# Optimization experiments

Measured on AMD Instinct MI355X. Metric: run time of the kernel, lower is better.

## Reference

```python
import jax, jax.numpy as jnp
import numpy as np

NUM_USER = 200000
NUM_QUESTION = 20000
NUM_CONCEPT = 128
DIM_HIDDEN = 512
BATCH = 16384


def _build_graph():
    # Deterministic DAG: edges go from lower to higher concept index, so
    # topological order is 0..C-1. Edge list is ordered by (to, from), so the
    # predecessors of node k occupy a contiguous slice of edge indices, matching
    # know_graph[know_graph['to']==k].sort_values(by='from').index.
    rng = np.random.RandomState(0)
    preds, offs, e = [], [], 0
    for k in range(NUM_CONCEPT):
        lp = 0 if k == 0 else int(rng.randint(0, min(k, 3) + 1))
        p = sorted(rng.choice(k, size=lp, replace=False).tolist()) if lp > 0 else []
        preds.append(p)
        offs.append(e)
        e += lp
    return preds, offs, e

PREDS, OFFS, NUM_EDGE = _build_graph()


def setup_inputs() -> dict:
    key = jax.random.key(0)
    ks = jax.random.split(key, 16)
    h2 = max(DIM_HIDDEN // 2, 1)
    inp = {
        'user_id': jax.random.randint(ks[0], (BATCH,), 0, NUM_USER),
        'question_id': jax.random.randint(ks[1], (BATCH,), 0, NUM_QUESTION),
        'priori': jax.random.normal(ks[2], (NUM_USER, NUM_CONCEPT), jnp.float32) * 0.1,
        'condi_p': jax.random.normal(ks[3], (NUM_USER, NUM_EDGE), jnp.float32) * 0.1,
        'condi_n': jax.random.normal(ks[4], (NUM_USER, NUM_EDGE), jnp.float32) * 0.1,
        'item_diff': jax.random.normal(ks[5], (NUM_QUESTION, NUM_CONCEPT), jnp.float32) * 0.1,
        'item_disc': jax.random.normal(ks[6], (NUM_QUESTION, 1), jnp.float32) * 0.1,
        'q_table': (jax.random.uniform(ks[7], (NUM_QUESTION, NUM_CONCEPT)) < 0.1).astype(jnp.float32),
        'Wu': jax.random.normal(ks[8], (DIM_HIDDEN, NUM_CONCEPT), jnp.float32) * 0.05,
        'bu': jnp.zeros((DIM_HIDDEN,), jnp.float32),
        'Wi': jax.random.normal(ks[9], (DIM_HIDDEN, NUM_CONCEPT), jnp.float32) * 0.05,
        'bi': jnp.zeros((DIM_HIDDEN,), jnp.float32),
        'W1': jax.random.normal(ks[10], (h2, DIM_HIDDEN), jnp.float32) * 0.05,
        'b1': jnp.zeros((h2,), jnp.float32),
        'W2': jax.random.normal(ks[11], (1, h2), jnp.float32) * 0.05,
        'b2': jnp.zeros((1,), jnp.float32),
    }
    return inp


def _posterior(user_id, priori, condi_p, condi_n):
    bp = jax.nn.sigmoid(priori[user_id])   # [B, C]
    bcp = jax.nn.sigmoid(condi_p[user_id])  # [B, E]
    bcn = jax.nn.sigmoid(condi_n[user_id])  # [B, E]
    post = [None] * NUM_CONCEPT
    for k in range(NUM_CONCEPT):
        preds = PREDS[k]
        lp = len(preds)
        if lp == 0:
            post[k] = bp[:, k]
            continue
        pr = jnp.stack([post[p] for p in preds], axis=1)          # [B, lp]
        cp = bcp[:, OFFS[k]:OFFS[k] + lp] ** (1.0 / lp)           # [B, lp]
        cn = bcn[:, OFFS[k]:OFFS[k] + lp] ** (1.0 / lp)
        # Exact closed form of the 2^lp mask sum: sum over binary masks of
        # prod_j(m_j*cp_j*pr_j + (1-m_j)*cn_j*(1-pr_j)) = prod_j(cp_j*pr_j + cn_j*(1-pr_j))
        post[k] = jnp.prod(cp * pr + cn * (1.0 - pr), axis=1)
    return jnp.stack(post, axis=1)  # [B, C]


def reference(user_id, question_id, priori, condi_p, condi_n, item_diff, item_disc,
              q_table, Wu, bu, Wi, bi, W1, b1, W2, b2):
    user_mastery = _posterior(user_id, priori, condi_p, condi_n)      # [B, C]
    diff = jax.nn.sigmoid(item_diff[question_id])                     # [B, C]
    disc = jax.nn.sigmoid(item_disc[question_id])                     # [B, 1]
    q = q_table[question_id]                                          # [B, C]
    user_factor = jnp.tanh((user_mastery * q) @ Wu.T + bu)            # [B, H]
    item_factor = jax.nn.sigmoid((diff * q) @ Wi.T + bi)              # [B, H]
    x = (user_factor - item_factor) * disc
    x = jax.nn.sigmoid(x @ W1.T + b1)
    x = jax.nn.sigmoid(x @ W2.T + b2)                                 # [B, 1]
    return jnp.squeeze(x, axis=-1)
```

## Files before the change

### kernel.cpp

```cpp
#include <hip/hip_runtime.h>
#include <hip/hip_bf16.h>
#include <stdint.h>

typedef __hip_bfloat16 bf16;

struct GraphArg {
  short offs[128];
  unsigned char lp[128];
  unsigned char preds[384];
  unsigned char elp[384];
};

namespace {
struct HostMT {
  uint32_t mt[624]; int pos;
  void seed(uint32_t s){
    mt[0]=s;
    for(int i=1;i<624;i++) mt[i]=1812433253u*(mt[i-1]^(mt[i-1]>>30))+(uint32_t)i;
    pos=624;
  }
  uint32_t next(){
    if(pos>=624){
      for(int i=0;i<624;i++){
        uint32_t y=(mt[i]&0x80000000u)|(mt[(i+1)%624]&0x7fffffffu);
        mt[i]=mt[(i+397)%624]^(y>>1)^((y&1u)?0x9908b0dfu:0u);
      }
      pos=0;
    }
    uint32_t y=mt[pos++];
    y^=y>>11; y^=(y<<7)&0x9d2c5680u; y^=(y<<15)&0xefc60000u; y^=y>>18;
    return y;
  }
  uint64_t next64(){ uint64_t hi=next(); uint64_t lo=next(); return (hi<<32)|lo; }
  uint32_t masked32(uint32_t rng){
    if(!rng) return 0u;
    uint32_t mask=rng; mask|=mask>>1; mask|=mask>>2; mask|=mask>>4; mask|=mask>>8; mask|=mask>>16;
    uint32_t v; do{ v=next()&mask; }while(v>rng); return v;
  }
  uint64_t masked64(uint64_t rng){
    if(!rng) return 0ull;
    uint64_t mask=rng; mask|=mask>>1; mask|=mask>>2; mask|=mask>>4; mask|=mask>>8; mask|=mask>>16; mask|=mask>>32;
    uint64_t v; do{ v=next64()&mask; }while(v>rng); return v;
  }
};

int build_graph(GraphArg& g, bool rand64, bool shuf64){
  HostMT st; st.seed(0u);
  for(int j=0;j<384;j++) g.elp[j]=0;
  int e=0; int perm[128];
  for(int k=0;k<128;k++){
    int l=0;
    if(k>0){
      uint32_t rng=(uint32_t)(k<3?k:3);
      l = rand64 ? (int)st.masked64(rng) : (int)st.masked32(rng);
    }
    g.offs[k]=(short)e; g.lp[k]=(unsigned char)l;
    g.preds[k*3]=0; g.preds[k*3+1]=0; g.preds[k*3+2]=0;
    if(l>0){
      for(int i=0;i<k;i++) perm[i]=i;
      for(int i=k-1;i>=1;i--){
        uint32_t j = shuf64 ? (uint32_t)st.masked64((uint64_t)i) : st.masked32((uint32_t)i);
        int t=perm[i]; perm[i]=perm[j]; perm[j]=t;
      }
      int sel[3]; for(int j=0;j<l;j++) sel[j]=perm[j];
      for(int a=1;a<l;a++){ int v=sel[a]; int b=a-1; while(b>=0&&sel[b]>v){sel[b+1]=sel[b];b--;} sel[b+1]=v; }
      for(int j=0;j<l;j++){ g.preds[k*3+j]=(unsigned char)sel[j]; g.elp[e+j]=(unsigned char)l; }
    }
    e+=l;
  }
  return e;
}
}

__device__ __forceinline__ float bf2f(bf16 v){ return __bfloat162float(v); }
__device__ __forceinline__ float sigmoidf_(float x){ return 1.0f/(1.0f+expf(-x)); }

template<bool F32> __device__ __forceinline__ float ld1(const void* p, long long i){
  if constexpr(F32) return ((const float*)p)[i];
  else return bf2f(((const bf16*)p)[i]);
}
template<bool F32> __device__ __forceinline__ void ld8(const void* p, long long i, float* f){
  if constexpr(F32){
    const float4* q = (const float4*)((const float*)p + i);
    float4 a=q[0], b=q[1];
    f[0]=a.x; f[1]=a.y; f[2]=a.z; f[3]=a.w; f[4]=b.x; f[5]=b.y; f[6]=b.z; f[7]=b.w;
  } else {
    union { uint4 u; unsigned short s[8]; } x;
    x.u = *reinterpret_cast<const uint4*>((const bf16*)p + i);
#pragma unroll
    for(int j=0;j<8;j++){ unsigned uu=((unsigned)x.s[j])<<16; float ff; __builtin_memcpy(&ff,&uu,4); f[j]=ff; }
  }
}
template<bool F32> __device__ __forceinline__ void st1(void* p, long long i, float v){
  if constexpr(F32) ((float*)p)[i]=v;
  else ((bf16*)p)[i]=__float2bfloat16(v);
}

__device__ __forceinline__ int pidx(int k,int e){ return (k<<4) + (e ^ (k&15)); }

template<bool F32>
__global__ __launch_bounds__(256) void fused(
    const int* __restrict__ user_id, const int* __restrict__ question_id,
    const void* __restrict__ priori, const void* __restrict__ condi_p, const void* __restrict__ condi_n,
    const void* __restrict__ item_diff, const void* __restrict__ item_disc, const void* __restrict__ q_table,
    const void* __restrict__ Wu, const void* __restrict__ bu,
    const void* __restrict__ Wi, const void* __restrict__ bi,
    const void* __restrict__ W1, const void* __restrict__ b1,
    const void* __restrict__ W2, const void* __restrict__ b2,
    void* __restrict__ out, long long E, long long maxCondi, GraphArg g)
{
  {
    const unsigned short* ph = (const unsigned short*)priori;
    int cnt=0;
#pragma unroll
    for(int i=0;i<64;i++){ unsigned ex=(ph[i]>>7)&0xFFu; cnt += (ex>=0x82u)?1:0; }
    const bool isF32 = (cnt>=4);
    if(isF32 != F32) return;
  }

  __shared__ __align__(16) char arena[40960];
  float* s_dq  =(float*)(arena);
  float* s_post=(float*)(arena+8192);
  float* s_cp  =(float*)(arena+16384);
  float* s_cn  =(float*)(arena+26880);
  float* s_mq  =(float*)(arena+16384);
  float* s_x   =(float*)(arena+24576);
  float* s_x1  =(float*)(arena+8192);

  const int tid=threadIdx.x;
  const long long b0=(long long)blockIdx.x*16;
  const int Ei=(int)E;
  const bool staged=(Ei>0 && Ei<=164);

  float qv[8];
#pragma unroll
  for(int it=0;it<8;++it){
    const int i=tid+(it<<8);
    const int e=i>>7, c=i&127;
    const int u=user_id[b0+e];
    s_post[pidx(c,e)]=sigmoidf_(ld1<F32>(priori,(long long)u*128+c));
    const int q=question_id[b0+e];
    const float qvv=ld1<F32>(q_table,(long long)q*128+c);
    qv[it]=qvv;
    s_dq[e*128+c]=sigmoidf_(ld1<F32>(item_diff,(long long)q*128+c))*qvv;
  }
  if(staged && tid<Ei){
    const int j=tid, lp=(int)g.elp[j];
    for(int e=0;e<16;e++){
      const int u=user_id[b0+e];
      const long long idx=(long long)u*E+j;
      float cp=sigmoidf_(ld1<F32>(condi_p,idx));
      float cn=sigmoidf_(ld1<F32>(condi_n,idx));
      if(lp==2){cp=sqrtf(cp);cn=sqrtf(cn);}
      else if(lp==3){cp=cbrtf(cp);cn=cbrtf(cn);}
      s_cp[e*Ei+j]=cp; s_cn[e*Ei+j]=cn;
    }
  }
  __syncthreads();

  if(tid<16){
    const int e=tid;
    if(staged){
      for(int k=0;k<128;k++){
        const int lp=(int)g.lp[k];
        if(lp==0) continue;
        const int off=(int)g.offs[k];
        float prod=1.0f;
        for(int j=0;j<lp;j++){
          const float pr=s_post[pidx((int)g.preds[k*3+j],e)];
          prod*=s_cp[e*Ei+off+j]*pr + s_cn[e*Ei+off+j]*(1.0f-pr);
        }
        s_post[pidx(k,e)]=prod;
      }
    } else {
      const int u=user_id[b0+e];
      const long long ubase=(long long)u*E;
      for(int k=0;k<128;k++){
        const int lp=(int)g.lp[k];
        if(lp==0) continue;
        const int off=(int)g.offs[k];
        float prod=1.0f;
        for(int j=0;j<lp;j++){
          long long idx=ubase+off+j; if(idx>maxCondi) idx=maxCondi;
          float bcp=sigmoidf_(ld1<F32>(condi_p,idx));
          float bcn=sigmoidf_(ld1<F32>(condi_n,idx));
          float cp,cn;
          if(lp==1){cp=bcp;cn=bcn;}
          else if(lp==2){cp=sqrtf(bcp);cn=sqrtf(bcn);}
          else {cp=cbrtf(bcp);cn=cbrtf(bcn);}
          const float pr=s_post[pidx((int)g.preds[k*3+j],e)];
          prod*=cp*pr+cn*(1.0f-pr);
        }
        s_post[pidx(k,e)]=prod;
      }
    }
  }
  __syncthreads();

#pragma unroll
  for(int it=0;it<8;++it){
    const int i=tid+(it<<8);
    const int e=i>>7, c=i&127;
    s_mq[e*128+c]=s_post[pidx(c,e)]*qv[it];
  }
  __syncthreads();

  for(int tile=0;tile<2;tile++){
    const int e0=tile*8;
    float dsc[8];
#pragma unroll
    for(int e=0;e<8;e++){
      const int q=question_id[b0+e0+e];
      dsc[e]=sigmoidf_(ld1<F32>(item_disc,q));
    }
    for(int half=0;half<2;half++){
      const int o=tid+half*256;
      float aU[8],aI[8];
#pragma unroll
      for(int e=0;e<8;e++){aU[e]=0.0f;aI[e]=0.0f;}
      for(int c=0;c<128;c+=8){
        float u8[8],i8[8];
        ld8<F32>(Wu,(long long)o*128+c,u8);
        ld8<F32>(Wi,(long long)o*128+c,i8);
#pragma unroll
        for(int e=0;e<8;e++){
          const float* m=&s_mq[(e0+e)*128+c];
          const float* d=&s_dq[(e0+e)*128+c];
#pragma unroll
          for(int j=0;j<8;j++){ aU[e]+=u8[j]*m[j]; aI[e]+=i8[j]*d[j]; }
        }
      }
      const float bou=ld1<F32>(bu,o), boi=ld1<F32>(bi,o);
#pragma unroll
      for(int e=0;e<8;e++){
        float uf=tanhf(aU[e]+bou);
        float fi=sigmoidf_(aI[e]+boi);
        s_x[e*512+o]=(uf-fi)*dsc[e];
      }
    }
    __syncthreads();
    {
      float a[8];
#pragma unroll
      for(int e=0;e<8;e++) a[e]=0.0f;
      for(int c=0;c<512;c+=8){
        float w8[8]; ld8<F32>(W1,(long long)tid*512+c,w8);
#pragma unroll
        for(int e=0;e<8;e++){
          const float* x=&s_x[e*512+c];
#pragma unroll
          for(int j=0;j<8;j++) a[e]+=w8[j]*x[j];
        }
      }
      const float bb=ld1<F32>(b1,tid);
#pragma unroll
      for(int e=0;e<8;e++) s_x1[e*256+tid]=sigmoidf_(a[e]+bb);
    }
    __syncthreads();
    {
      const int e=tid>>5, l=tid&31;
      float a=0.0f;
      for(int h=l;h<256;h+=32) a+=s_x1[e*256+h]*ld1<F32>(W2,h);
      for(int off=16;off>0;off>>=1) a+=__shfl_down(a,off,32);
      if(l==0) st1<F32>(out,b0+e0+e,sigmoidf_(a+ld1<F32>(b2,0)));
    }
    __syncthreads();
  }
}

extern "C" void kernel_launch(void* const* d_in, const int* in_sizes, int n_in,
                              void* d_out, int out_size, void* d_ws, size_t ws_size,
                              hipStream_t stream) {
  const int* user_id     = (const int*)d_in[0];
  const int* question_id = (const int*)d_in[1];
  const void* priori     = d_in[2];
  const void* condi_p    = d_in[3];
  const void* condi_n    = d_in[4];
  const void* item_diff  = d_in[5];
  const void* item_disc  = d_in[6];
  const void* q_table    = d_in[7];
  const void* Wu = d_in[8];  const void* bu = d_in[9];
  const void* Wi = d_in[10]; const void* bi = d_in[11];
  const void* W1 = d_in[12]; const void* b1 = d_in[13];
  const void* W2 = d_in[14]; const void* b2 = d_in[15];
  (void)n_in; (void)out_size; (void)d_ws; (void)ws_size;

  const int batch    = in_sizes[0];
  const int num_user = in_sizes[2] / 128;
  const long long E  = in_sizes[3] / num_user;
  const long long maxCondi = (long long)num_user * E - 1;

  GraphArg g;
  int e_tot = build_graph(g, false, false);
  if(e_tot != (int)E) e_tot = build_graph(g, true,  false);
  if(e_tot != (int)E) e_tot = build_graph(g, false, true);
  if(e_tot != (int)E) e_tot = build_graph(g, true,  true);
  if(e_tot != (int)E) (void)build_graph(g, false, false);

  const int blocks = batch / 16;
  fused<false><<<blocks,256,0,stream>>>(user_id,question_id,priori,condi_p,condi_n,
      item_diff,item_disc,q_table,Wu,bu,Wi,bi,W1,b1,W2,b2,d_out,E,maxCondi,g);
  fused<true ><<<blocks,256,0,stream>>>(user_id,question_id,priori,condi_p,condi_n,
      item_diff,item_disc,q_table,Wu,bu,Wi,bi,W1,b1,W2,b2,d_out,E,maxCondi,g);
}
```

Measured before the change: 935.7 us.

## Process 32 batch rows per block and restructure shared-memory staging

Each block now handles 32 samples instead of 16, so the posterior recurrence runs on 32 lanes and the weight loads for Wu/Wi/W1 are reused across four 8-row tiles instead of two. The shared-memory arena grows to about 57KB with a new layout: the swizzled posterior index is replaced by a plain c*32+e layout, and the q_table/item_diff/item_disc loads move after the posterior phase. This halves the block count and raises shared memory per block, which may lower occupancy and parallelism across CUs.

New measurement: 757.3 us. -19.1%, faster.

```diff
diff --git a/kernel.cpp b/kernel.cpp
--- a/kernel.cpp
+++ b/kernel.cpp
@@ -95,8 +95,6 @@
   if constexpr(F32) ((float*)p)[i]=v;
   else ((bf16*)p)[i]=__float2bfloat16(v);
 }
-
-__device__ __forceinline__ int pidx(int k,int e){ return (k<<4) + (e ^ (k&15)); }
 
 template<bool F32>
 __global__ __launch_bounds__(256) void fused(
@@ -118,35 +116,29 @@
     if(isF32 != F32) return;
   }
 
-  __shared__ __align__(16) char arena[40960];
-  float* s_dq  =(float*)(arena);
-  float* s_post=(float*)(arena+8192);
+  __shared__ __align__(16) char arena[58368];
+  float* s_post=(float*)(arena);
+  float* s_x   =(float*)(arena);
+  float* s_x1  =(float*)(arena+16384);
   float* s_cp  =(float*)(arena+16384);
-  float* s_cn  =(float*)(arena+26880);
-  float* s_mq  =(float*)(arena+16384);
-  float* s_x   =(float*)(arena+24576);
-  float* s_x1  =(float*)(arena+8192);
+  float* s_disc=(float*)(arena+24576);
+  float* s_mq  =(float*)(arena+25600);
+  float* s_cn  =(float*)(arena+37376);
+  float* s_dq  =(float*)(arena+41984);
 
   const int tid=threadIdx.x;
-  const long long b0=(long long)blockIdx.x*16;
+  const long long b0=(long long)blockIdx.x*32;
   const int Ei=(int)E;
   const bool staged=(Ei>0 && Ei<=164);
 
-  float qv[8];
-#pragma unroll
-  for(int it=0;it<8;++it){
-    const int i=tid+(it<<8);
+  for(int i=tid;i<32*128;i+=256){
     const int e=i>>7, c=i&127;
     const int u=user_id[b0+e];
-    s_post[pidx(c,e)]=sigmoidf_(ld1<F32>(priori,(long long)u*128+c));
-    const int q=question_id[b0+e];
-    const float qvv=ld1<F32>(q_table,(long long)q*128+c);
-    qv[it]=qvv;
-    s_dq[e*128+c]=sigmoidf_(ld1<F32>(item_diff,(long long)q*128+c))*qvv;
+    s_post[c*32+e]=sigmoidf_(ld1<F32>(priori,(long long)u*128+c));
   }
   if(staged && tid<Ei){
     const int j=tid, lp=(int)g.elp[j];
-    for(int e=0;e<16;e++){
+    for(int e=0;e<32;e++){
       const int u=user_id[b0+e];
       const long long idx=(long long)u*E+j;
       float cp=sigmoidf_(ld1<F32>(condi_p,idx));
@@ -158,7 +150,7 @@
   }
   __syncthreads();
 
-  if(tid<16){
+  if(tid<32){
     const int e=tid;
     if(staged){
       for(int k=0;k<128;k++){
@@ -167,10 +159,10 @@
         const int off=(int)g.offs[k];
         float prod=1.0f;
         for(int j=0;j<lp;j++){
-          const float pr=s_post[pidx((int)g.preds[k*3+j],e)];
+          const float pr=s_post[(int)g.preds[k*3+j]*32+e];
           prod*=s_cp[e*Ei+off+j]*pr + s_cn[e*Ei+off+j]*(1.0f-pr);
         }
-        s_post[pidx(k,e)]=prod;
+        s_post[k*32+e]=prod;
       }
     } else {
       const int u=user_id[b0+e];
@@ -188,31 +180,27 @@
           if(lp==1){cp=bcp;cn=bcn;}
           else if(lp==2){cp=sqrtf(bcp);cn=sqrtf(bcn);}
           else {cp=cbrtf(bcp);cn=cbrtf(bcn);}
-          const float pr=s_post[pidx((int)g.preds[k*3+j],e)];
+          const float pr=s_post[(int)g.preds[k*3+j]*32+e];
           prod*=cp*pr+cn*(1.0f-pr);
         }
-        s_post[pidx(k,e)]=prod;
+        s_post[k*32+e]=prod;
       }
     }
   }
   __syncthreads();
 
-#pragma unroll
-  for(int it=0;it<8;++it){
-    const int i=tid+(it<<8);
+  for(int i=tid;i<32*128;i+=256){
     const int e=i>>7, c=i&127;
-    s_mq[e*128+c]=s_post[pidx(c,e)]*qv[it];
+    const int q=question_id[b0+e];
+    const float qv=ld1<F32>(q_table,(long long)q*128+c);
+    s_mq[e*128+c]=s_post[c*32+e]*qv;
+    s_dq[e*128+c]=sigmoidf_(ld1<F32>(item_diff,(long long)q*128+c))*qv;
+    if(c==0) s_disc[e]=sigmoidf_(ld1<F32>(item_disc,q));
   }
   __syncthreads();
 
-  for(int tile=0;tile<2;tile++){
+  for(int tile=0;tile<4;tile++){
     const int e0=tile*8;
-    float dsc[8];
-#pragma unroll
-    for(int e=0;e<8;e++){
-      const int q=question_id[b0+e0+e];
-      dsc[e]=sigmoidf_(ld1<F32>(item_disc,q));
-    }
     for(int half=0;half<2;half++){
       const int o=tid+half*256;
       float aU[8],aI[8];
@@ -235,7 +223,7 @@
       for(int e=0;e<8;e++){
         float uf=tanhf(aU[e]+bou);
         float fi=sigmoidf_(aI[e]+boi);
-        s_x[e*512+o]=(uf-fi)*dsc[e];
+        s_x[e*512+o]=(uf-fi)*s_disc[e0+e];
       }
     }
     __syncthreads();
@@ -297,7 +285,7 @@
   if(e_tot != (int)E) e_tot = build_graph(g, true,  true);
   if(e_tot != (int)E) (void)build_graph(g, false, false);
 
-  const int blocks = batch / 16;
+  const int blocks = batch / 32;
   fused<false><<<blocks,256,0,stream>>>(user_id,question_id,priori,condi_p,condi_n,
       item_diff,item_disc,q_table,Wu,bu,Wi,bi,W1,b1,W2,b2,d_out,E,maxCondi,g);
   fused<true ><<<blocks,256,0,stream>>>(user_id,question_id,priori,condi_p,condi_n,
```
